# Kernel tuning notes

Measured on AMD Instinct MI355X. Metric: run time of the kernel, lower is better.

## Reference

```python
import jax, jax.numpy as jnp
import numpy as np
from jax import lax

N_USERS, N_ITEMS = 40000, 60000
N = N_USERS + N_ITEMS
D = 64
E = 800000
L = 2
BIAS = 1e-4
AUTO_T = 1.0


def setup_inputs() -> dict:
    key = jax.random.key(0)
    ks = jax.random.split(key, 12)
    emb0 = jax.random.normal(ks[0], (N, D), dtype=jnp.float32) * 0.1
    h_idx = jax.random.randint(ks[1], (E,), 0, N)
    t_idx = jax.random.randint(ks[2], (E,), 0, N)
    # symmetric normalization G = D^-1/2 A D^-1/2 (values share A's sparsity)
    deg = jax.ops.segment_sum(jnp.ones((E,), jnp.float32), h_idx, num_segments=N)
    dis = jnp.where(deg > 0, deg ** -0.5, 0.0)
    G_values = dis[h_idx] * dis[t_idx]
    # Gumbel noise: -log(-log(U(bias, 1-bias)))
    ue = jax.random.uniform(ks[3], (L, E), minval=BIAS, maxval=1.0 - BIAS)
    edge_gumbel = -jnp.log(-jnp.log(ue))
    un = jax.random.uniform(ks[4], (L, N, D), minval=BIAS, maxval=1.0 - BIAS)
    emb_gumbel = -jnp.log(-jnp.log(un))
    sc2, sc1 = (2.0 / (3 * D)) ** 0.5, (2.0 / (2 * D)) ** 0.5
    edge_W1 = jax.random.normal(ks[5], (L, 2 * D, D), dtype=jnp.float32) * sc2
    edge_b1 = jnp.zeros((L, D), jnp.float32)
    edge_W2 = jax.random.normal(ks[6], (L, D, 1), dtype=jnp.float32) * sc1
    edge_b2 = jnp.zeros((L, 1), jnp.float32)
    emb_W1 = jax.random.normal(ks[7], (L, D, D), dtype=jnp.float32) * sc1
    emb_b1 = jnp.zeros((L, D), jnp.float32)
    emb_W2 = jax.random.normal(ks[8], (L, D, D), dtype=jnp.float32) * sc1
    emb_b2 = jnp.zeros((L, D), jnp.float32)
    return dict(emb0=emb0, h_idx=h_idx, t_idx=t_idx, G_values=G_values,
                edge_gumbel=edge_gumbel, emb_gumbel=emb_gumbel,
                edge_W1=edge_W1, edge_b1=edge_b1, edge_W2=edge_W2, edge_b2=edge_b2,
                emb_W1=emb_W1, emb_b1=emb_b1, emb_W2=emb_W2, emb_b2=emb_b2)


def _spmm(vals, h, t, x, n):
    # out[h] += vals * x[t]
    return jax.ops.segment_sum(vals[:, None] * x[t], h, num_segments=n)


def reference(emb0, h_idx, t_idx, G_values, edge_gumbel, emb_gumbel,
              edge_W1, edge_b1, edge_W2, edge_b2,
              emb_W1, emb_b1, emb_W2, emb_b2):
    n = emb0.shape[0]
    e0 = e1 = e2 = emb0
    s0 = s1 = s2 = emb0
    for i in range(edge_W1.shape[0]):
        # branch 0: plain normalized propagation
        gnn0 = _spmm(G_values, h_idx, t_idx, e0, n)
        # branch 1: learned edge reweighting (auto_augment_s, is_norm=True)
        edge_emb = jnp.concatenate([e1[h_idx], e1[t_idx]], axis=1)      # [E, 2D]
        logits = jnp.maximum(edge_emb @ edge_W1[i] + edge_b1[i], 0.0) @ edge_W2[i] + edge_b2[i]  # [E,1]
        w = jax.nn.sigmoid((edge_gumbel[i][:, None] + logits) / AUTO_T)[:, 0]
        w = lax.stop_gradient(w)                                         # detached in original
        row = jax.ops.segment_sum(w, h_idx, num_segments=n)
        dinv = jnp.where(row > 0, 1.0 / row, 0.0)                        # pow(-1).nan_to_num(0)
        vals1 = dinv[h_idx] * w
        gnn1 = _spmm(vals1, h_idx, t_idx, e1, n)
        # branch 2: learned feature gating (auto_augment_f)
        lg = jnp.maximum(e2 @ emb_W1[i] + emb_b1[i], 0.0) @ emb_W2[i] + emb_b2[i]
        gate = lax.stop_gradient(jax.nn.sigmoid((emb_gumbel[i] + lg) / AUTO_T))
        gnn2 = _spmm(G_values, h_idx, t_idx, gate * e2, n)
        e0 = gnn0 + e0
        e1 = gnn1 + e1
        e2 = gnn2 + e2
        s0 = s0 + e0
        s1 = s1 + e1
        s2 = s2 + e2
    return jnp.stack([s0, s1, s2])  # [3, N, D]; split rows into users/items downstream
```

## Files before the change

### kernel.cpp

```cpp
#include <hip/hip_runtime.h>
#include <hip/hip_bf16.h>
#include <math.h>

#define ST_E 68
#define ST_W 68
#define ST_WX 132

#define PK_STRIDE 256

typedef float v4f __attribute__((ext_vector_type(4)));

__device__ __forceinline__ float4 f4z() { return make_float4(0.f, 0.f, 0.f, 0.f); }
__device__ __forceinline__ void fma4(float4& a, float s, const float4& v) {
  a.x = fmaf(s, v.x, a.x); a.y = fmaf(s, v.y, a.y);
  a.z = fmaf(s, v.z, a.z); a.w = fmaf(s, v.w, a.w);
}
__device__ __forceinline__ float4 add4(const float4& a, const float4& b) {
  return make_float4(a.x + b.x, a.y + b.y, a.z + b.z, a.w + b.w);
}
__device__ __forceinline__ void stnt4(float* p, const float4& v) {
  v4f u; u.x = v.x; u.y = v.y; u.z = v.z; u.w = v.w;
  __builtin_nontemporal_store(u, (v4f*)p);
}
__device__ __forceinline__ float4 lo4(const uint4& u) {
  float4 f;
  f.x = __uint_as_float(u.x << 16);
  f.y = __uint_as_float(u.x & 0xffff0000u);
  f.z = __uint_as_float(u.y << 16);
  f.w = __uint_as_float(u.y & 0xffff0000u);
  return f;
}
__device__ __forceinline__ float4 hi4(const uint4& u) {
  float4 f;
  f.x = __uint_as_float(u.z << 16);
  f.y = __uint_as_float(u.z & 0xffff0000u);
  f.z = __uint_as_float(u.w << 16);
  f.w = __uint_as_float(u.w & 0xffff0000u);
  return f;
}
__device__ __forceinline__ float4 ldbf4(const unsigned short* p) {
  ushort4 u = *(const ushort4*)p;
  float4 f;
  f.x = __uint_as_float((unsigned)u.x << 16);
  f.y = __uint_as_float((unsigned)u.y << 16);
  f.z = __uint_as_float((unsigned)u.z << 16);
  f.w = __uint_as_float((unsigned)u.w << 16);
  return f;
}
__device__ __forceinline__ unsigned short f2bf(float v) {
  __hip_bfloat16 h = __float2bfloat16(v);
  return *reinterpret_cast<unsigned short*>(&h);
}
__device__ __forceinline__ unsigned pack2(float a, float b) {
  return ((unsigned)f2bf(b) << 16) | (unsigned)f2bf(a);
}
__device__ __forceinline__ void st4bf(unsigned short* p, const float4& v) {
  ushort4 u;
  u.x = f2bf(v.x); u.y = f2bf(v.y); u.z = f2bf(v.z); u.w = f2bf(v.w);
  *(ushort4*)p = u;
}
__device__ __forceinline__ float fsig(float x) {
  return __builtin_amdgcn_rcpf(1.f + __expf(-x));
}

__global__ void init_k(const float* __restrict__ emb0, unsigned short* __restrict__ pk0,
                       unsigned short* __restrict__ e2b, int N) {
  int idx = blockIdx.x * blockDim.x + threadIdx.x;
  int n = idx >> 4, q = idx & 15;
  if (n >= N) return;
  float4 v = *(const float4*)(emb0 + (size_t)n * 64 + q * 4);
  unsigned p01 = pack2(v.x, v.y), p23 = pack2(v.z, v.w);
  uint4 u = make_uint4(p01, p23, p01, p23);
  *(uint4*)(pk0 + (size_t)n * PK_STRIDE + q * 8) = u;
  st4bf(e2b + (size_t)n * 64 + q * 4, v);
}

__global__ void hist_k(const int* __restrict__ h, int* __restrict__ deg, int E) {
  int i = blockIdx.x * blockDim.x + threadIdx.x;
  if (i < E) atomicAdd(&deg[h[i]], 1);
}

__global__ void scanA_k(const int* __restrict__ deg, int* __restrict__ rp,
                        int* __restrict__ sums, int N) {
  __shared__ int s[1024];
  int i = blockIdx.x * 1024 + threadIdx.x;
  int v = (i < N) ? deg[i] : 0;
  s[threadIdx.x] = v;
  __syncthreads();
  for (int off = 1; off < 1024; off <<= 1) {
    int t = (threadIdx.x >= (unsigned)off) ? s[threadIdx.x - off] : 0;
    __syncthreads();
    s[threadIdx.x] += t;
    __syncthreads();
  }
  if (i < N) rp[i] = s[threadIdx.x] - v;
  if (threadIdx.x == 1023) sums[blockIdx.x] = s[1023];
}

__global__ void scanB_k(int* sums, int nch) {
  int lane = threadIdx.x;
  int run = 0;
  for (int base = 0; base < nch; base += 64) {
    int v = (base + lane < nch) ? sums[base + lane] : 0;
    int incl = v;
    for (int off = 1; off < 64; off <<= 1) {
      int t = __shfl_up(incl, off, 64);
      if (lane >= off) incl += t;
    }
    if (base + lane < nch) sums[base + lane] = run + (incl - v);
    run += __shfl(incl, 63, 64);
  }
}

__global__ void scanC_k(int* __restrict__ rp, int* __restrict__ cur,
                        const int* __restrict__ sums, int N, int E) {
  int i = blockIdx.x * blockDim.x + threadIdx.x;
  if (i < N) {
    int v = rp[i] + sums[i >> 10];
    rp[i] = v; cur[i] = v;
  } else if (i == N) {
    rp[N] = E;
  }
}

__global__ void fill_k(const int* __restrict__ h, const int* __restrict__ t_idx,
                       const float* __restrict__ G, const float* __restrict__ gum,
                       int* __restrict__ cur, int4* __restrict__ emeta,
                       float* __restrict__ cgum, int E, int L) {
  int i = blockIdx.x * blockDim.x + threadIdx.x;
  if (i < E) {
    int pos = atomicAdd(&cur[h[i]], 1);
    int4 em;
    em.x = t_idx[i] * PK_STRIDE;
    em.y = __float_as_int(G[i]);
    em.z = __float_as_int(gum[i]);
    em.w = (L > 1) ? __float_as_int(gum[(size_t)E + i]) : 0;
    emeta[pos] = em;
    if (L > 2)
      for (int l = 2; l < L; l++) cgum[(size_t)l * E + pos] = gum[(size_t)l * E + i];
  }
}

__global__ __launch_bounds__(256) void xht_k(const unsigned short* __restrict__ pkin,
                                             const float* __restrict__ W,
                                             unsigned short* __restrict__ xhb,
                                             unsigned short* __restrict__ pk, int N) {
  __shared__ float et[64 * ST_E];
  __shared__ float wl[64 * ST_WX];
  int tid = threadIdx.x;
  int n0 = blockIdx.x * 64;
  for (int i = tid; i < 64 * 16; i += 256) {
    int r = i >> 4, c = i & 15;
    float4 v = f4z();
    if (n0 + r < N) {
      uint4 u = *(const uint4*)(pkin + (size_t)(n0 + r) * PK_STRIDE + c * 8);
      v = hi4(u);
    }
    *(float4*)(et + r * ST_E + c * 4) = v;
  }
  for (int i = tid; i < 128 * 16; i += 256) {
    int r = i >> 4, c4 = (i & 15) * 4;
    float4 v = *(const float4*)(W + r * 64 + c4);
    if (r < 64) *(float4*)(wl + r * ST_WX + c4) = v;
    else        *(float4*)(wl + (r - 64) * ST_WX + 64 + c4) = v;
  }
  __syncthreads();
  int rg = tid >> 4, tx = tid & 15;
  int s2 = (tx >> 2) * 2;
  float acc[4][8];
#pragma unroll
  for (int i = 0; i < 4; i++)
#pragma unroll
    for (int j = 0; j < 8; j++) acc[i][j] = 0.f;
#pragma unroll 4
  for (int k = 0; k < 64; k++) {
    int kk = (k + s2) & 63;
    float a0 = et[(rg * 4 + 0) * ST_E + kk];
    float a1 = et[(rg * 4 + 1) * ST_E + kk];
    float a2 = et[(rg * 4 + 2) * ST_E + kk];
    float a3 = et[(rg * 4 + 3) * ST_E + kk];
    float4 b0 = *(const float4*)(wl + kk * ST_WX + tx * 4);
    float4 b1 = *(const float4*)(wl + kk * ST_WX + 64 + tx * 4);
    acc[0][0] = fmaf(a0, b0.x, acc[0][0]); acc[0][1] = fmaf(a0, b0.y, acc[0][1]);
    acc[0][2] = fmaf(a0, b0.z, acc[0][2]); acc[0][3] = fmaf(a0, b0.w, acc[0][3]);
    acc[0][4] = fmaf(a0, b1.x, acc[0][4]); acc[0][5] = fmaf(a0, b1.y, acc[0][5]);
    acc[0][6] = fmaf(a0, b1.z, acc[0][6]); acc[0][7] = fmaf(a0, b1.w, acc[0][7]);
    acc[1][0] = fmaf(a1, b0.x, acc[1][0]); acc[1][1] = fmaf(a1, b0.y, acc[1][1]);
    acc[1][2] = fmaf(a1, b0.z, acc[1][2]); acc[1][3] = fmaf(a1, b0.w, acc[1][3]);
    acc[1][4] = fmaf(a1, b1.x, acc[1][4]); acc[1][5] = fmaf(a1, b1.y, acc[1][5]);
    acc[1][6] = fmaf(a1, b1.z, acc[1][6]); acc[1][7] = fmaf(a1, b1.w, acc[1][7]);
    acc[2][0] = fmaf(a2, b0.x, acc[2][0]); acc[2][1] = fmaf(a2, b0.y, acc[2][1]);
    acc[2][2] = fmaf(a2, b0.z, acc[2][2]); acc[2][3] = fmaf(a2, b0.w, acc[2][3]);
    acc[2][4] = fmaf(a2, b1.x, acc[2][4]); acc[2][5] = fmaf(a2, b1.y, acc[2][5]);
    acc[2][6] = fmaf(a2, b1.z, acc[2][6]); acc[2][7] = fmaf(a2, b1.w, acc[2][7]);
    acc[3][0] = fmaf(a3, b0.x, acc[3][0]); acc[3][1] = fmaf(a3, b0.y, acc[3][1]);
    acc[3][2] = fmaf(a3, b0.z, acc[3][2]); acc[3][3] = fmaf(a3, b0.w, acc[3][3]);
    acc[3][4] = fmaf(a3, b1.x, acc[3][4]); acc[3][5] = fmaf(a3, b1.y, acc[3][5]);
    acc[3][6] = fmaf(a3, b1.z, acc[3][6]); acc[3][7] = fmaf(a3, b1.w, acc[3][7]);
  }
#pragma unroll
  for (int i = 0; i < 4; i++) {
    int n = n0 + rg * 4 + i;
    if (n < N) {
      st4bf(xhb + (size_t)n * 64 + tx * 4,
            make_float4(acc[i][0], acc[i][1], acc[i][2], acc[i][3]));
      st4bf(pk + (size_t)n * PK_STRIDE + 128 + tx * 8 + 4,
            make_float4(acc[i][4], acc[i][5], acc[i][6], acc[i][7]));
    }
  }
}

__global__ __launch_bounds__(256) void mlp2_k(const unsigned short* __restrict__ e2b,
    const float* __restrict__ W1, const float* __restrict__ b1,
    const float* __restrict__ W2, const float* __restrict__ b2,
    const float* __restrict__ gum, unsigned short* __restrict__ pk, int N) {
  __shared__ float et[64 * ST_E];
  __shared__ float w1l[64 * ST_W];
  __shared__ float w2l[64 * ST_W];
  __shared__ float ht[64 * ST_E];
  int tid = threadIdx.x;
  int n0 = blockIdx.x * 64;
  for (int i = tid; i < 64 * 16; i += 256) {
    int r = i >> 4, c4 = (i & 15) * 4;
    float4 v = (n0 + r < N) ? ldbf4(e2b + (size_t)(n0 + r) * 64 + c4) : f4z();
    *(float4*)(et + r * ST_E + c4) = v;
    *(float4*)(w1l + r * ST_W + c4) = *(const float4*)(W1 + r * 64 + c4);
    *(float4*)(w2l + r * ST_W + c4) = *(const float4*)(W2 + r * 64 + c4);
  }
  __syncthreads();
  int rg = tid >> 4, tx = tid & 15;
  int s2 = (tx >> 2) * 2;
  float acc[4][4];
#pragma unroll
  for (int i = 0; i < 4; i++)
#pragma unroll
    for (int j = 0; j < 4; j++) acc[i][j] = 0.f;
#pragma unroll 4
  for (int k = 0; k < 64; k++) {
    int kk = (k + s2) & 63;
    float a0 = et[(rg * 4 + 0) * ST_E + kk];
    float a1 = et[(rg * 4 + 1) * ST_E + kk];
    float a2 = et[(rg * 4 + 2) * ST_E + kk];
    float a3 = et[(rg * 4 + 3) * ST_E + kk];
    float4 bv = *(const float4*)(w1l + kk * ST_W + tx * 4);
    acc[0][0] = fmaf(a0, bv.x, acc[0][0]); acc[0][1] = fmaf(a0, bv.y, acc[0][1]);
    acc[0][2] = fmaf(a0, bv.z, acc[0][2]); acc[0][3] = fmaf(a0, bv.w, acc[0][3]);
    acc[1][0] = fmaf(a1, bv.x, acc[1][0]); acc[1][1] = fmaf(a1, bv.y, acc[1][1]);
    acc[1][2] = fmaf(a1, bv.z, acc[1][2]); acc[1][3] = fmaf(a1, bv.w, acc[1][3]);
    acc[2][0] = fmaf(a2, bv.x, acc[2][0]); acc[2][1] = fmaf(a2, bv.y, acc[2][1]);
    acc[2][2] = fmaf(a2, bv.z, acc[2][2]); acc[2][3] = fmaf(a2, bv.w, acc[2][3]);
    acc[3][0] = fmaf(a3, bv.x, acc[3][0]); acc[3][1] = fmaf(a3, bv.y, acc[3][1]);
    acc[3][2] = fmaf(a3, bv.z, acc[3][2]); acc[3][3] = fmaf(a3, bv.w, acc[3][3]);
  }
  float4 b1v = *(const float4*)(b1 + tx * 4);
#pragma unroll
  for (int i = 0; i < 4; i++) {
    float4 hv = make_float4(fmaxf(acc[i][0] + b1v.x, 0.f), fmaxf(acc[i][1] + b1v.y, 0.f),
                            fmaxf(acc[i][2] + b1v.z, 0.f), fmaxf(acc[i][3] + b1v.w, 0.f));
    *(float4*)(ht + (rg * 4 + i) * ST_E + tx * 4) = hv;
  }
  __syncthreads();
  float acc2[4][4];
#pragma unroll
  for (int i = 0; i < 4; i++)
#pragma unroll
    for (int j = 0; j < 4; j++) acc2[i][j] = 0.f;
#pragma unroll 4
  for (int k = 0; k < 64; k++) {
    int kk = (k + s2) & 63;
    float a0 = ht[(rg * 4 + 0) * ST_E + kk];
    float a1 = ht[(rg * 4 + 1) * ST_E + kk];
    float a2 = ht[(rg * 4 + 2) * ST_E + kk];
    float a3 = ht[(rg * 4 + 3) * ST_E + kk];
    float4 bv = *(const float4*)(w2l + kk * ST_W + tx * 4);
    acc2[0][0] = fmaf(a0, bv.x, acc2[0][0]); acc2[0][1] = fmaf(a0, bv.y, acc2[0][1]);
    acc2[0][2] = fmaf(a0, bv.z, acc2[0][2]); acc2[0][3] = fmaf(a0, bv.w, acc2[0][3]);
    acc2[1][0] = fmaf(a1, bv.x, acc2[1][0]); acc2[1][1] = fmaf(a1, bv.y, acc2[1][1]);
    acc2[1][2] = fmaf(a1, bv.z, acc2[1][2]); acc2[1][3] = fmaf(a1, bv.w, acc2[1][3]);
    acc2[2][0] = fmaf(a2, bv.x, acc2[2][0]); acc2[2][1] = fmaf(a2, bv.y, acc2[2][1]);
    acc2[2][2] = fmaf(a2, bv.z, acc2[2][2]); acc2[2][3] = fmaf(a2, bv.w, acc2[2][3]);
    acc2[3][0] = fmaf(a3, bv.x, acc2[3][0]); acc2[3][1] = fmaf(a3, bv.y, acc2[3][1]);
    acc2[3][2] = fmaf(a3, bv.z, acc2[3][2]); acc2[3][3] = fmaf(a3, bv.w, acc2[3][3]);
  }
  float4 b2v = *(const float4*)(b2 + tx * 4);
#pragma unroll
  for (int i = 0; i < 4; i++) {
    int n = n0 + rg * 4 + i;
    if (n < N) {
      float4 gv = *(const float4*)(gum + (size_t)n * 64 + tx * 4);
      float4 ev = *(const float4*)(et + (rg * 4 + i) * ST_E + tx * 4);
      float4 yv;
      yv.x = ev.x * fsig(gv.x + acc2[i][0] + b2v.x);
      yv.y = ev.y * fsig(gv.y + acc2[i][1] + b2v.y);
      yv.z = ev.z * fsig(gv.z + acc2[i][2] + b2v.z);
      yv.w = ev.w * fsig(gv.w + acc2[i][3] + b2v.w);
      st4bf(pk + (size_t)n * PK_STRIDE + 128 + tx * 8, yv);
    }
  }
}

#define CH 2

#define LOADCH(Abuf, Bbuf, I0)                                          \
  _Pragma("unroll")                                                     \
  for (int c = 0; c < CH; c++) {                                        \
    int i_ = (I0) + c;                                                  \
    int tof_ = __shfl(em.x, i_ & 15, 16);                               \
    if (i_ < cnt) {                                                     \
      const unsigned short* pr_ = pk + (size_t)tof_ + l * 8;            \
      Abuf[c] = *(const uint4*)(pr_);                                   \
      Bbuf[c] = *(const uint4*)(pr_ + 128);                             \
    }                                                                   \
  }

#define COMPCH(Abuf, Bbuf, I0)                                          \
  _Pragma("unroll")                                                     \
  for (int c = 0; c < CH; c++) {                                        \
    int i_ = (I0) + c;                                                  \
    float gg_ = __shfl(__int_as_float(em.y), i_ & 15, 16);              \
    float gu_ = __shfl(guv, i_ & 15, 16);                               \
    if (i_ < cnt) {                                                     \
      float4 v0_ = lo4(Abuf[c]);                                        \
      float4 v1_ = hi4(Abuf[c]);                                        \
      float4 vy_ = lo4(Bbuf[c]);                                        \
      float4 xt_ = hi4(Bbuf[c]);                                        \
      float pq_ = fmaxf(xb1.x + xt_.x, 0.f) * w2v.x                     \
                + fmaxf(xb1.y + xt_.y, 0.f) * w2v.y                     \
                + fmaxf(xb1.z + xt_.z, 0.f) * w2v.z                     \
                + fmaxf(xb1.w + xt_.w, 0.f) * w2v.w;                    \
      pq_ += __shfl_xor(pq_, 1, 16);                                    \
      pq_ += __shfl_xor(pq_, 2, 16);                                    \
      pq_ += __shfl_xor(pq_, 4, 16);                                    \
      pq_ += __shfl_xor(pq_, 8, 16);                                    \
      float w_ = fsig(gu_ + pq_ + b2s);                                 \
      wsum += w_;                                                       \
      fma4(acc0, gg_, v0_);                                             \
      fma4(acc1, w_, v1_);                                              \
      fma4(acc2, gg_, vy_);                                             \
    }                                                                   \
  }

template <int FIRST, int OUTM, int GSEL>
__global__ __launch_bounds__(256) void spmm3f_k(const int* __restrict__ rp,
    const int4* __restrict__ emeta, const float* __restrict__ cgum,
    const unsigned short* __restrict__ pk, const unsigned short* __restrict__ xhb,
    const unsigned short* __restrict__ e2b_in,
    const float* __restrict__ b1, const float* __restrict__ W2,
    const float* __restrict__ b2, const float* __restrict__ emb0,
    unsigned short* __restrict__ pkn, unsigned short* __restrict__ e2b,
    float* __restrict__ out0, float* __restrict__ out1, float* __restrict__ out2,
    int N) {
  int g = threadIdx.x >> 4;
  int l = threadIdx.x & 15;
  int n = blockIdx.x * 16 + g;
  if (n >= N) return;
  int jb = rp[n], je = rp[n + 1];
  size_t o64 = (size_t)n * 64 + l * 4;
  float4 xh4 = ldbf4(xhb + o64);
  float4 b1v = *(const float4*)(b1 + l * 4);
  float4 xb1 = add4(xh4, b1v);
  float4 w2v = *(const float4*)(W2 + l * 4);
  float b2s = b2[0];
  float4 rc0, rc1, rc2;
  if (FIRST) {
    rc0 = *(const float4*)(emb0 + o64);
    rc1 = rc0; rc2 = rc0;
  } else {
    uint4 rA = *(const uint4*)(pk + (size_t)n * PK_STRIDE + l * 8);
    rc0 = lo4(rA);
    rc1 = hi4(rA);
    rc2 = ldbf4(e2b_in + o64);
  }
  float4 acc0 = f4z(), acc1 = f4z(), acc2 = f4z();
  float wsum = 0.f;
  for (int base = jb; base < je; base += 16) {
    int idx = base + l;
    bool valid = idx < je;
    int4 em = valid ? emeta[idx] : make_int4(0, 0, 0, 0);
    float guv;
    if (GSEL == 0) guv = __int_as_float(em.z);
    else if (GSEL == 1) guv = __int_as_float(em.w);
    else guv = valid ? cgum[idx] : 0.f;
    int cnt = min(16, je - base);
    uint4 A0[CH], B0[CH], A1[CH], B1[CH];
    LOADCH(A0, B0, 0)
    for (int i0 = 0; i0 < cnt; i0 += 2 * CH) {
      LOADCH(A1, B1, i0 + CH)
      COMPCH(A0, B0, i0)
      LOADCH(A0, B0, i0 + 2 * CH)
      COMPCH(A1, B1, i0 + CH)
    }
  }
  float dinv = (wsum > 0.f) ? __builtin_amdgcn_rcpf(wsum) : 0.f;
  float4 en0 = add4(acc0, rc0);
  acc1.x *= dinv; acc1.y *= dinv; acc1.z *= dinv; acc1.w *= dinv;
  float4 en1 = add4(acc1, rc1);
  float4 en2 = add4(acc2, rc2);
  if (OUTM != 1) {
    uint4 wA;
    wA.x = pack2(en0.x, en0.y); wA.y = pack2(en0.z, en0.w);
    wA.z = pack2(en1.x, en1.y); wA.w = pack2(en1.z, en1.w);
    *(uint4*)(pkn + (size_t)n * PK_STRIDE + l * 8) = wA;
    st4bf(e2b + o64, en2);
  }
  if (OUTM == 1) {
    float4 base = *(const float4*)(emb0 + o64);
    stnt4(out0 + o64, add4(base, add4(rc0, en0)));
    stnt4(out1 + o64, add4(base, add4(rc1, en1)));
    stnt4(out2 + o64, add4(base, add4(rc2, en2)));
  } else if (OUTM == 2) {
    *(float4*)(out0 + o64) = add4(rc0, en0);
    *(float4*)(out1 + o64) = add4(rc1, en1);
    *(float4*)(out2 + o64) = add4(rc2, en2);
  } else if (OUTM == 3) {
    *(float4*)(out0 + o64) = add4(*(const float4*)(out0 + o64), en0);
    *(float4*)(out1 + o64) = add4(*(const float4*)(out1 + o64), en1);
    *(float4*)(out2 + o64) = add4(*(const float4*)(out2 + o64), en2);
  }
}

extern "C" void kernel_launch(void* const* d_in, const int* in_sizes, int n_in,
                              void* d_out, int out_size, void* d_ws, size_t ws_size,
                              hipStream_t stream) {
  const float* emb0        = (const float*)d_in[0];
  const int*   h_idx       = (const int*)d_in[1];
  const int*   t_idx       = (const int*)d_in[2];
  const float* G_values    = (const float*)d_in[3];
  const float* edge_gumbel = (const float*)d_in[4];
  const float* emb_gumbel  = (const float*)d_in[5];
  const float* edge_W1     = (const float*)d_in[6];
  const float* edge_b1     = (const float*)d_in[7];
  const float* edge_W2     = (const float*)d_in[8];
  const float* edge_b2     = (const float*)d_in[9];
  const float* emb_W1      = (const float*)d_in[10];
  const float* emb_b1      = (const float*)d_in[11];
  const float* emb_W2      = (const float*)d_in[12];
  const float* emb_b2      = (const float*)d_in[13];

  const int D = 64;
  const int N = in_sizes[0] / D;
  const int E = in_sizes[1];
  const int L = in_sizes[4] / E;
  const size_t ND = (size_t)N * D;

  char* p = (char*)d_ws;
  auto alloc = [&](size_t bytes) -> char* {
    char* r = p;
    p += (bytes + 255) & ~(size_t)255;
    return r;
  };
  unsigned short* xhb = (unsigned short*)alloc(ND * 2);
  unsigned short* e2b = (unsigned short*)alloc(ND * 2);
  unsigned short* pkA = (unsigned short*)alloc((size_t)N * PK_STRIDE * 2);
  unsigned short* pkB = (unsigned short*)alloc((size_t)N * PK_STRIDE * 2);
  int4*  emeta = (int4*)alloc((size_t)E * 16);
  float* cgum  = (float*)alloc((size_t)L * E * 4);
  int*   deg   = (int*)alloc((size_t)N * 4);
  int*   cur   = (int*)alloc((size_t)N * 4);
  int*   rp    = (int*)alloc(((size_t)N + 1) * 4);
  int*   sums  = (int*)alloc(1024 * 4);

  float* out = (float*)d_out;

  init_k<<<(N * 16 + 255) / 256, 256, 0, stream>>>(emb0, pkA, e2b, N);
  hipMemsetAsync(deg, 0, (size_t)N * 4, stream);
  hist_k<<<(E + 255) / 256, 256, 0, stream>>>(h_idx, deg, E);
  int nch = (N + 1023) / 1024;
  scanA_k<<<nch, 1024, 0, stream>>>(deg, rp, sums, N);
  scanB_k<<<1, 64, 0, stream>>>(sums, nch);
  scanC_k<<<(N + 256) / 256, 256, 0, stream>>>(rp, cur, sums, N, E);
  fill_k<<<(E + 255) / 256, 256, 0, stream>>>(h_idx, t_idx, G_values, edge_gumbel,
                                              cur, emeta, cgum, E, L);

  int nb64 = (N + 63) / 64;
  int nb16 = (N + 15) / 16;

  for (int i = 0; i < L; i++) {
    unsigned short* pkc = (i & 1) ? pkB : pkA;
    unsigned short* pkn = (i & 1) ? pkA : pkB;
    xht_k<<<nb64, 256, 0, stream>>>(pkc, edge_W1 + (size_t)i * 128 * 64, xhb, pkc, N);
    mlp2_k<<<nb64, 256, 0, stream>>>(e2b, emb_W1 + (size_t)i * 4096,
                                     emb_b1 + (size_t)i * 64,
                                     emb_W2 + (size_t)i * 4096,
                                     emb_b2 + (size_t)i * 64,
                                     emb_gumbel + (size_t)i * ND, pkc, N);
    const float* cg = cgum + (size_t)i * E;
    const float* eb1 = edge_b1 + (size_t)i * 64;
    const float* eW2 = edge_W2 + (size_t)i * 64;
    const float* eb2 = edge_b2 + i;
    if (L == 2) {
      if (i == 0)
        spmm3f_k<1, 0, 0><<<nb16, 256, 0, stream>>>(rp, emeta, cg, pkc, xhb, e2b,
                                                    eb1, eW2, eb2, emb0, pkn, e2b,
                                                    out, out + ND, out + 2 * ND, N);
      else
        spmm3f_k<0, 1, 1><<<nb16, 256, 0, stream>>>(rp, emeta, cg, pkc, xhb, e2b,
                                                    eb1, eW2, eb2, emb0, pkn, e2b,
                                                    out, out + ND, out + 2 * ND, N);
    } else {
      if (i == 0)
        spmm3f_k<1, 2, 2><<<nb16, 256, 0, stream>>>(rp, emeta, cg, pkc, xhb, e2b,
                                                    eb1, eW2, eb2, emb0, pkn, e2b,
                                                    out, out + ND, out + 2 * ND, N);
      else
        spmm3f_k<0, 3, 2><<<nb16, 256, 0, stream>>>(rp, emeta, cg, pkc, xhb, e2b,
                                                    eb1, eW2, eb2, emb0, pkn, e2b,
                                                    out, out + ND, out + 2 * ND, N);
    }
  }
}
```

Measured before the change: 410.0 us.

## Fuse edge and feature-gate dense GEMMs into one MFMA bf16 kernel

Replaces the two scalar-FMA dense kernels (edge projection and the two-layer gating MLP) with a single kernel that runs all three 64-wide GEMMs on bf16 MFMA 16x16x32 instructions. A new prep kernel converts the weights to transposed bf16 layout once per call. Operands are staged in shared memory as bf16 rather than fp32, and the hidden activations reuse a shared buffer. This removes one launch and the FMA-bound inner loops. In exchange the hidden layer is rounded to bf16 and outputs are written as scattered 2-byte stores.

```diff
diff --git a/kernel.cpp b/kernel.cpp
--- a/kernel.cpp
+++ b/kernel.cpp
@@ -2,13 +2,12 @@
 #include <hip/hip_bf16.h>
 #include <math.h>
 
-#define ST_E 68
-#define ST_W 68
-#define ST_WX 132
-
 #define PK_STRIDE 256
+#define LDA 72
 
 typedef float v4f __attribute__((ext_vector_type(4)));
+typedef __attribute__((ext_vector_type(8))) short s8;
+typedef __attribute__((ext_vector_type(4))) float f4;
 
 __device__ __forceinline__ float4 f4z() { return make_float4(0.f, 0.f, 0.f, 0.f); }
 __device__ __forceinline__ void fma4(float4& a, float s, const float4& v) {
@@ -141,160 +140,134 @@
   }
 }
 
-__global__ __launch_bounds__(256) void xht_k(const unsigned short* __restrict__ pkin,
-                                             const float* __restrict__ W,
-                                             unsigned short* __restrict__ xhb,
-                                             unsigned short* __restrict__ pk, int N) {
-  __shared__ float et[64 * ST_E];
-  __shared__ float wl[64 * ST_WX];
+__global__ void wprep_k(const float* __restrict__ edge_W1,
+                        const float* __restrict__ emb_W1,
+                        const float* __restrict__ emb_W2,
+                        unsigned short* __restrict__ wxT,
+                        unsigned short* __restrict__ w1T,
+                        unsigned short* __restrict__ w2T, int L) {
+  const int per = 128 * 64 + 64 * 64 + 64 * 64;
+  int i = blockIdx.x * blockDim.x + threadIdx.x;
+  if (i >= L * per) return;
+  int layer = i / per, r = i % per;
+  if (r < 8192) {
+    int j = r >> 6, k = r & 63;
+    float v = (j < 64) ? edge_W1[((size_t)layer * 128 + k) * 64 + j]
+                       : edge_W1[((size_t)layer * 128 + 64 + k) * 64 + (j - 64)];
+    wxT[(size_t)layer * 8192 + j * 64 + k] = f2bf(v);
+  } else if (r < 8192 + 4096) {
+    int q = r - 8192; int n = q >> 6, k = q & 63;
+    w1T[(size_t)layer * 4096 + n * 64 + k] =
+        f2bf(emb_W1[((size_t)layer * 64 + k) * 64 + n]);
+  } else {
+    int q = r - 12288; int n = q >> 6, k = q & 63;
+    w2T[(size_t)layer * 4096 + n * 64 + k] =
+        f2bf(emb_W2[((size_t)layer * 64 + k) * 64 + n]);
+  }
+}
+
+__global__ __launch_bounds__(256) void dense_k(
+    const unsigned short* __restrict__ pkin,
+    const unsigned short* __restrict__ e2b,
+    const unsigned short* __restrict__ wxT,
+    const unsigned short* __restrict__ w1T,
+    const unsigned short* __restrict__ w2T,
+    const float* __restrict__ b1,
+    const float* __restrict__ b2,
+    const float* __restrict__ gum,
+    unsigned short* __restrict__ xhb,
+    unsigned short* __restrict__ pk,
+    int N) {
+  __shared__ unsigned short a1[64 * LDA];
+  __shared__ unsigned short a2[64 * LDA];
+  __shared__ unsigned short wx[128 * LDA];
+  __shared__ unsigned short w1[64 * LDA];
+  __shared__ unsigned short w2[64 * LDA];
   int tid = threadIdx.x;
   int n0 = blockIdx.x * 64;
   for (int i = tid; i < 64 * 16; i += 256) {
     int r = i >> 4, c = i & 15;
-    float4 v = f4z();
+    ushort4 v1 = make_ushort4(0, 0, 0, 0), v2 = v1;
     if (n0 + r < N) {
-      uint4 u = *(const uint4*)(pkin + (size_t)(n0 + r) * PK_STRIDE + c * 8);
-      v = hi4(u);
-    }
-    *(float4*)(et + r * ST_E + c * 4) = v;
-  }
-  for (int i = tid; i < 128 * 16; i += 256) {
-    int r = i >> 4, c4 = (i & 15) * 4;
-    float4 v = *(const float4*)(W + r * 64 + c4);
-    if (r < 64) *(float4*)(wl + r * ST_WX + c4) = v;
-    else        *(float4*)(wl + (r - 64) * ST_WX + 64 + c4) = v;
+      v1 = *(const ushort4*)(pkin + (size_t)(n0 + r) * PK_STRIDE + c * 8 + 4);
+      v2 = *(const ushort4*)(e2b + (size_t)(n0 + r) * 64 + c * 4);
+    }
+    *(ushort4*)(a1 + r * LDA + c * 4) = v1;
+    *(ushort4*)(a2 + r * LDA + c * 4) = v2;
+  }
+  for (int i = tid; i < 128 * 8; i += 256) {
+    int r = i >> 3, s = i & 7;
+    *(uint4*)(wx + r * LDA + s * 8) = *(const uint4*)(wxT + r * 64 + s * 8);
+  }
+  for (int i = tid; i < 64 * 8; i += 256) {
+    int r = i >> 3, s = i & 7;
+    *(uint4*)(w1 + r * LDA + s * 8) = *(const uint4*)(w1T + r * 64 + s * 8);
+    *(uint4*)(w2 + r * LDA + s * 8) = *(const uint4*)(w2T + r * 64 + s * 8);
   }
   __syncthreads();
-  int rg = tid >> 4, tx = tid & 15;
-  int s2 = (tx >> 2) * 2;
-  float acc[4][8];
-#pragma unroll
-  for (int i = 0; i < 4; i++)
-#pragma unroll
-    for (int j = 0; j < 8; j++) acc[i][j] = 0.f;
-#pragma unroll 4
-  for (int k = 0; k < 64; k++) {
-    int kk = (k + s2) & 63;
-    float a0 = et[(rg * 4 + 0) * ST_E + kk];
-    float a1 = et[(rg * 4 + 1) * ST_E + kk];
-    float a2 = et[(rg * 4 + 2) * ST_E + kk];
-    float a3 = et[(rg * 4 + 3) * ST_E + kk];
-    float4 b0 = *(const float4*)(wl + kk * ST_WX + tx * 4);
-    float4 b1 = *(const float4*)(wl + kk * ST_WX + 64 + tx * 4);
-    acc[0][0] = fmaf(a0, b0.x, acc[0][0]); acc[0][1] = fmaf(a0, b0.y, acc[0][1]);
-    acc[0][2] = fmaf(a0, b0.z, acc[0][2]); acc[0][3] = fmaf(a0, b0.w, acc[0][3]);
-    acc[0][4] = fmaf(a0, b1.x, acc[0][4]); acc[0][5] = fmaf(a0, b1.y, acc[0][5]);
-    acc[0][6] = fmaf(a0, b1.z, acc[0][6]); acc[0][7] = fmaf(a0, b1.w, acc[0][7]);
-    acc[1][0] = fmaf(a1, b0.x, acc[1][0]); acc[1][1] = fmaf(a1, b0.y, acc[1][1]);
-    acc[1][2] = fmaf(a1, b0.z, acc[1][2]); acc[1][3] = fmaf(a1, b0.w, acc[1][3]);
-    acc[1][4] = fmaf(a1, b1.x, acc[1][4]); acc[1][5] = fmaf(a1, b1.y, acc[1][5]);
-    acc[1][6] = fmaf(a1, b1.z, acc[1][6]); acc[1][7] = fmaf(a1, b1.w, acc[1][7]);
-    acc[2][0] = fmaf(a2, b0.x, acc[2][0]); acc[2][1] = fmaf(a2, b0.y, acc[2][1]);
-    acc[2][2] = fmaf(a2, b0.z, acc[2][2]); acc[2][3] = fmaf(a2, b0.w, acc[2][3]);
-    acc[2][4] = fmaf(a2, b1.x, acc[2][4]); acc[2][5] = fmaf(a2, b1.y, acc[2][5]);
-    acc[2][6] = fmaf(a2, b1.z, acc[2][6]); acc[2][7] = fmaf(a2, b1.w, acc[2][7]);
-    acc[3][0] = fmaf(a3, b0.x, acc[3][0]); acc[3][1] = fmaf(a3, b0.y, acc[3][1]);
-    acc[3][2] = fmaf(a3, b0.z, acc[3][2]); acc[3][3] = fmaf(a3, b0.w, acc[3][3]);
-    acc[3][4] = fmaf(a3, b1.x, acc[3][4]); acc[3][5] = fmaf(a3, b1.y, acc[3][5]);
-    acc[3][6] = fmaf(a3, b1.z, acc[3][6]); acc[3][7] = fmaf(a3, b1.w, acc[3][7]);
-  }
-#pragma unroll
-  for (int i = 0; i < 4; i++) {
-    int n = n0 + rg * 4 + i;
-    if (n < N) {
-      st4bf(xhb + (size_t)n * 64 + tx * 4,
-            make_float4(acc[i][0], acc[i][1], acc[i][2], acc[i][3]));
-      st4bf(pk + (size_t)n * PK_STRIDE + 128 + tx * 8 + 4,
-            make_float4(acc[i][4], acc[i][5], acc[i][6], acc[i][7]));
-    }
-  }
-}
-
-__global__ __launch_bounds__(256) void mlp2_k(const unsigned short* __restrict__ e2b,
-    const float* __restrict__ W1, const float* __restrict__ b1,
-    const float* __restrict__ W2, const float* __restrict__ b2,
-    const float* __restrict__ gum, unsigned short* __restrict__ pk, int N) {
-  __shared__ float et[64 * ST_E];
-  __shared__ float w1l[64 * ST_W];
-  __shared__ float w2l[64 * ST_W];
-  __shared__ float ht[64 * ST_E];
-  int tid = threadIdx.x;
-  int n0 = blockIdx.x * 64;
-  for (int i = tid; i < 64 * 16; i += 256) {
-    int r = i >> 4, c4 = (i & 15) * 4;
-    float4 v = (n0 + r < N) ? ldbf4(e2b + (size_t)(n0 + r) * 64 + c4) : f4z();
-    *(float4*)(et + r * ST_E + c4) = v;
-    *(float4*)(w1l + r * ST_W + c4) = *(const float4*)(W1 + r * 64 + c4);
-    *(float4*)(w2l + r * ST_W + c4) = *(const float4*)(W2 + r * 64 + c4);
-  }
-  __syncthreads();
-  int rg = tid >> 4, tx = tid & 15;
-  int s2 = (tx >> 2) * 2;
-  float acc[4][4];
-#pragma unroll
-  for (int i = 0; i < 4; i++)
-#pragma unroll
-    for (int j = 0; j < 4; j++) acc[i][j] = 0.f;
-#pragma unroll 4
-  for (int k = 0; k < 64; k++) {
-    int kk = (k + s2) & 63;
-    float a0 = et[(rg * 4 + 0) * ST_E + kk];
-    float a1 = et[(rg * 4 + 1) * ST_E + kk];
-    float a2 = et[(rg * 4 + 2) * ST_E + kk];
-    float a3 = et[(rg * 4 + 3) * ST_E + kk];
-    float4 bv = *(const float4*)(w1l + kk * ST_W + tx * 4);
-    acc[0][0] = fmaf(a0, bv.x, acc[0][0]); acc[0][1] = fmaf(a0, bv.y, acc[0][1]);
-    acc[0][2] = fmaf(a0, bv.z, acc[0][2]); acc[0][3] = fmaf(a0, bv.w, acc[0][3]);
-    acc[1][0] = fmaf(a1, bv.x, acc[1][0]); acc[1][1] = fmaf(a1, bv.y, acc[1][1]);
-    acc[1][2] = fmaf(a1, bv.z, acc[1][2]); acc[1][3] = fmaf(a1, bv.w, acc[1][3]);
-    acc[2][0] = fmaf(a2, bv.x, acc[2][0]); acc[2][1] = fmaf(a2, bv.y, acc[2][1]);
-    acc[2][2] = fmaf(a2, bv.z, acc[2][2]); acc[2][3] = fmaf(a2, bv.w, acc[2][3]);
-    acc[3][0] = fmaf(a3, bv.x, acc[3][0]); acc[3][1] = fmaf(a3, bv.y, acc[3][1]);
-    acc[3][2] = fmaf(a3, bv.z, acc[3][2]); acc[3][3] = fmaf(a3, bv.w, acc[3][3]);
-  }
-  float4 b1v = *(const float4*)(b1 + tx * 4);
-#pragma unroll
-  for (int i = 0; i < 4; i++) {
-    float4 hv = make_float4(fmaxf(acc[i][0] + b1v.x, 0.f), fmaxf(acc[i][1] + b1v.y, 0.f),
-                            fmaxf(acc[i][2] + b1v.z, 0.f), fmaxf(acc[i][3] + b1v.w, 0.f));
-    *(float4*)(ht + (rg * 4 + i) * ST_E + tx * 4) = hv;
-  }
-  __syncthreads();
-  float acc2[4][4];
-#pragma unroll
-  for (int i = 0; i < 4; i++)
-#pragma unroll
-    for (int j = 0; j < 4; j++) acc2[i][j] = 0.f;
-#pragma unroll 4
-  for (int k = 0; k < 64; k++) {
-    int kk = (k + s2) & 63;
-    float a0 = ht[(rg * 4 + 0) * ST_E + kk];
-    float a1 = ht[(rg * 4 + 1) * ST_E + kk];
-    float a2 = ht[(rg * 4 + 2) * ST_E + kk];
-    float a3 = ht[(rg * 4 + 3) * ST_E + kk];
-    float4 bv = *(const float4*)(w2l + kk * ST_W + tx * 4);
-    acc2[0][0] = fmaf(a0, bv.x, acc2[0][0]); acc2[0][1] = fmaf(a0, bv.y, acc2[0][1]);
-    acc2[0][2] = fmaf(a0, bv.z, acc2[0][2]); acc2[0][3] = fmaf(a0, bv.w, acc2[0][3]);
-    acc2[1][0] = fmaf(a1, bv.x, acc2[1][0]); acc2[1][1] = fmaf(a1, bv.y, acc2[1][1]);
-    acc2[1][2] = fmaf(a1, bv.z, acc2[1][2]); acc2[1][3] = fmaf(a1, bv.w, acc2[1][3]);
-    acc2[2][0] = fmaf(a2, bv.x, acc2[2][0]); acc2[2][1] = fmaf(a2, bv.y, acc2[2][1]);
-    acc2[2][2] = fmaf(a2, bv.z, acc2[2][2]); acc2[2][3] = fmaf(a2, bv.w, acc2[2][3]);
-    acc2[3][0] = fmaf(a3, bv.x, acc2[3][0]); acc2[3][1] = fmaf(a3, bv.y, acc2[3][1]);
-    acc2[3][2] = fmaf(a3, bv.z, acc2[3][2]); acc2[3][3] = fmaf(a3, bv.w, acc2[3][3]);
-  }
-  float4 b2v = *(const float4*)(b2 + tx * 4);
-#pragma unroll
-  for (int i = 0; i < 4; i++) {
-    int n = n0 + rg * 4 + i;
-    if (n < N) {
-      float4 gv = *(const float4*)(gum + (size_t)n * 64 + tx * 4);
-      float4 ev = *(const float4*)(et + (rg * 4 + i) * ST_E + tx * 4);
-      float4 yv;
-      yv.x = ev.x * fsig(gv.x + acc2[i][0] + b2v.x);
-      yv.y = ev.y * fsig(gv.y + acc2[i][1] + b2v.y);
-      yv.z = ev.z * fsig(gv.z + acc2[i][2] + b2v.z);
-      yv.w = ev.w * fsig(gv.w + acc2[i][3] + b2v.w);
-      st4bf(pk + (size_t)n * PK_STRIDE + 128 + tx * 8, yv);
+  int wv = tid >> 6, l = tid & 63;
+  int l15 = l & 15, lg = l >> 4;
+  int wr = wv * 16;
+  int arow = wr + l15;
+  s8 af1_0 = *(const s8*)(a1 + arow * LDA + 8 * lg);
+  s8 af1_1 = *(const s8*)(a1 + arow * LDA + 32 + 8 * lg);
+#pragma unroll
+  for (int ct = 0; ct < 8; ct++) {
+    f4 acc = {0.f, 0.f, 0.f, 0.f};
+    s8 b0 = *(const s8*)(wx + (ct * 16 + l15) * LDA + 8 * lg);
+    s8 bI = *(const s8*)(wx + (ct * 16 + l15) * LDA + 32 + 8 * lg);
+    acc = __builtin_amdgcn_mfma_f32_16x16x32_bf16(af1_0, b0, acc, 0, 0, 0);
+    acc = __builtin_amdgcn_mfma_f32_16x16x32_bf16(af1_1, bI, acc, 0, 0, 0);
+#pragma unroll
+    for (int j = 0; j < 4; j++) {
+      int n = n0 + wr + lg * 4 + j;
+      if (n < N) {
+        if (ct < 4) {
+          xhb[(size_t)n * 64 + ct * 16 + l15] = f2bf(acc[j]);
+        } else {
+          int c2 = (ct - 4) * 16 + l15;
+          pk[(size_t)n * PK_STRIDE + 128 + (c2 >> 2) * 8 + 4 + (c2 & 3)] = f2bf(acc[j]);
+        }
+      }
+    }
+  }
+  s8 af2_0 = *(const s8*)(a2 + arow * LDA + 8 * lg);
+  s8 af2_1 = *(const s8*)(a2 + arow * LDA + 32 + 8 * lg);
+#pragma unroll
+  for (int ct = 0; ct < 4; ct++) {
+    f4 acc = {0.f, 0.f, 0.f, 0.f};
+    s8 b0 = *(const s8*)(w1 + (ct * 16 + l15) * LDA + 8 * lg);
+    s8 bI = *(const s8*)(w1 + (ct * 16 + l15) * LDA + 32 + 8 * lg);
+    acc = __builtin_amdgcn_mfma_f32_16x16x32_bf16(af2_0, b0, acc, 0, 0, 0);
+    acc = __builtin_amdgcn_mfma_f32_16x16x32_bf16(af2_1, bI, acc, 0, 0, 0);
+    float bb = b1[ct * 16 + l15];
+#pragma unroll
+    for (int j = 0; j < 4; j++) {
+      float h = fmaxf(acc[j] + bb, 0.f);
+      a1[(wr + lg * 4 + j) * LDA + ct * 16 + l15] = f2bf(h);
+    }
+  }
+  s8 afh_0 = *(const s8*)(a1 + arow * LDA + 8 * lg);
+  s8 afh_1 = *(const s8*)(a1 + arow * LDA + 32 + 8 * lg);
+#pragma unroll
+  for (int ct = 0; ct < 4; ct++) {
+    f4 acc = {0.f, 0.f, 0.f, 0.f};
+    s8 b0 = *(const s8*)(w2 + (ct * 16 + l15) * LDA + 8 * lg);
+    s8 bI = *(const s8*)(w2 + (ct * 16 + l15) * LDA + 32 + 8 * lg);
+    acc = __builtin_amdgcn_mfma_f32_16x16x32_bf16(afh_0, b0, acc, 0, 0, 0);
+    acc = __builtin_amdgcn_mfma_f32_16x16x32_bf16(afh_1, bI, acc, 0, 0, 0);
+    int c2 = ct * 16 + l15;
+    float bb = b2[c2];
+#pragma unroll
+    for (int j = 0; j < 4; j++) {
+      int row = wr + lg * 4 + j;
+      int n = n0 + row;
+      if (n < N) {
+        float gv = gum[(size_t)n * 64 + c2];
+        float e2v = __uint_as_float((unsigned)a2[row * LDA + c2] << 16);
+        float y = e2v * fsig(gv + acc[j] + bb);
+        pk[(size_t)n * PK_STRIDE + 128 + (c2 >> 2) * 8 + (c2 & 3)] = f2bf(y);
+      }
     }
   }
 }
@@ -455,6 +428,9 @@
   unsigned short* pkB = (unsigned short*)alloc((size_t)N * PK_STRIDE * 2);
   int4*  emeta = (int4*)alloc((size_t)E * 16);
   float* cgum  = (float*)alloc((size_t)L * E * 4);
+  unsigned short* wxT = (unsigned short*)alloc((size_t)L * 8192 * 2);
+  unsigned short* w1T = (unsigned short*)alloc((size_t)L * 4096 * 2);
+  unsigned short* w2T = (unsigned short*)alloc((size_t)L * 4096 * 2);
   int*   deg   = (int*)alloc((size_t)N * 4);
   int*   cur   = (int*)alloc((size_t)N * 4);
   int*   rp    = (int*)alloc(((size_t)N + 1) * 4);
@@ -471,6 +447,8 @@
   scanC_k<<<(N + 256) / 256, 256, 0, stream>>>(rp, cur, sums, N, E);
   fill_k<<<(E + 255) / 256, 256, 0, stream>>>(h_idx, t_idx, G_values, edge_gumbel,
                                               cur, emeta, cgum, E, L);
+  wprep_k<<<(L * 16384 + 255) / 256, 256, 0, stream>>>(edge_W1, emb_W1, emb_W2,
+                                                       wxT, w1T, w2T, L);
 
   int nb64 = (N + 63) / 64;
   int nb16 = (N + 15) / 16;
@@ -478,12 +456,14 @@
   for (int i = 0; i < L; i++) {
     unsigned short* pkc = (i & 1) ? pkB : pkA;
     unsigned short* pkn = (i & 1) ? pkA : pkB;
-    xht_k<<<nb64, 256, 0, stream>>>(pkc, edge_W1 + (size_t)i * 128 * 64, xhb, pkc, N);
-    mlp2_k<<<nb64, 256, 0, stream>>>(e2b, emb_W1 + (size_t)i * 4096,
-                                     emb_b1 + (size_t)i * 64,
-                                     emb_W2 + (size_t)i * 4096,
-                                     emb_b2 + (size_t)i * 64,
-                                     emb_gumbel + (size_t)i * ND, pkc, N);
+    dense_k<<<nb64, 256, 0, stream>>>(pkc, e2b,
+                                      wxT + (size_t)i * 8192,
+                                      w1T + (size_t)i * 4096,
+                                      w2T + (size_t)i * 4096,
+                                      emb_b1 + (size_t)i * 64,
+                                      emb_b2 + (size_t)i * 64,
+                                      emb_gumbel + (size_t)i * ND,
+                                      xhb, pkc, N);
     const float* cg = cgum + (size_t)i * E;
     const float* eb1 = edge_b1 + (size_t)i * 64;
     const float* eW2 = edge_W2 + (size_t)i * 64;
```

Result: faster. 346.3 us (-15.5%).
